# Kernel tuning notes

Measured on AMD Instinct MI355X. Metric: run time of the kernel, lower is better.

The kernel has to match this reference:

```python
import jax, jax.numpy as jnp
import numpy as np

H = 51  # num_hidden

def lstm_cell(x, h, c, Wih, Whh, bih, bhh):
    # PyTorch LSTMCell gate order: i, f, g, o
    gates = x @ Wih.T + bih + h @ Whh.T + bhh
    i, f, g, o = jnp.split(gates, 4, axis=-1)
    c_new = jax.nn.sigmoid(f) * c + jax.nn.sigmoid(i) * jnp.tanh(g)
    h_new = jax.nn.sigmoid(o) * jnp.tanh(c_new)
    return h_new, c_new

def setup_inputs() -> dict:
    key = jax.random.key(0)
    ks = jax.random.split(key, 9)
    B, T = 8192, 512
    s1 = 1.0 / np.sqrt(H)  # torch LSTMCell init scale U(-1/sqrt(H), 1/sqrt(H))
    s2 = 1.0
    u = lambda k, shape, s: jax.random.uniform(k, shape, jnp.float32, -s, s)
    return {
        "x": jax.random.normal(ks[0], (B, T), dtype=jnp.float32),
        "Wih1": u(ks[1], (4 * H, 1), s1),
        "Whh1": u(ks[2], (4 * H, H), s1),
        "bih1": u(ks[3], (4 * H,), s1),
        "bhh1": u(ks[4], (4 * H,), s1),
        "Wih2": u(ks[5], (4, H), s2),
        "Whh2": u(ks[6], (4, 1), s2),
        "bih2": u(ks[7], (4,), s2),
        "bhh2": u(ks[8], (4,), s2),
    }

def reference(x, Wih1, Whh1, bih1, bhh1, Wih2, Whh2, bih2, bhh2):
    B, T = x.shape
    xs = x.T[:, :, None]  # [T, B, 1]
    h1 = jnp.zeros((B, H), x.dtype)
    c1 = jnp.zeros((B, H), x.dtype)
    h2 = jnp.zeros((B, 1), x.dtype)
    c2 = jnp.zeros((B, 1), x.dtype)

    def step(carry, xt):
        h1, c1, h2, c2 = carry
        h1, c1 = lstm_cell(xt, h1, c1, Wih1, Whh1, bih1, bhh1)
        h2, c2 = lstm_cell(c1, h2, c2, Wih2, Whh2, bih2, bhh2)
        return (h1, c1, h2, c2), None

    (h1, c1, h2, c2), _ = jax.lax.scan(step, (h1, c1, h2, c2), xs)
    # extra step after the loop (as in the original forward)
    h1, c1 = lstm_cell(c2, h1, c1, Wih1, Whh1, bih1, bhh1)
    h2, output = lstm_cell(c1, h2, c2, Wih2, Whh2, bih2, bhh2)
    return output  # [B, 1] (final cell state of lstm2)
```

## Files before the change

### kernel.cpp

```cpp
#include <hip/hip_runtime.h>

#define TT 512
#define L2E  1.4426950408889634f
#define L2E2 2.8853900817779268f

typedef _Float16 f16;
typedef _Float16 f16x8 __attribute__((ext_vector_type(8)));
typedef float f32x4 __attribute__((ext_vector_type(4)));

__device__ __forceinline__ float fsig_p(float a){
    return __builtin_amdgcn_rcpf(1.f + __builtin_amdgcn_exp2f(-a));
}
__device__ __forceinline__ float ftanhg_p(float a){
    return 2.f * __builtin_amdgcn_rcpf(1.f + __builtin_amdgcn_exp2f(-a)) - 1.f;
}
__device__ __forceinline__ float ftanh_c(float c){
    return 2.f * __builtin_amdgcn_rcpf(1.f + __builtin_amdgcn_exp2f(-L2E2*c)) - 1.f;
}

#define FMA_LO(accv, wd, hh) asm("v_fma_mix_f32 %0, %1, %2, %0 op_sel:[0,0,0] op_sel_hi:[1,0,0]" : "+v"(accv) : "v"(wd), "v"(hh))
#define FMA_HI(accv, wd, hh) asm("v_fma_mix_f32 %0, %1, %2, %0 op_sel:[1,0,0] op_sel_hi:[1,0,0]" : "+v"(accv) : "v"(wd), "v"(hh))

__global__ void repack_w(const float* __restrict__ Whh1, const float* __restrict__ Wih1,
                         const float* __restrict__ bih1, const float* __restrict__ bhh1,
                         const float* __restrict__ Wih2,
                         f16* __restrict__ Wp, f16* __restrict__ Wp2)
{
    int i = blockIdx.x*256 + threadIdx.x;
    if (i < 13*2*64*8) {
        int b    = i & 7;
        int lane = (i >> 3) & 63;
        int kt   = (i >> 9) & 1;
        int m    = i >> 10;
        int r = m*16 + (lane & 15);
        int u = r >> 2, g = r & 3;
        int k = kt*32 + (lane >> 4)*8 + b;
        float v = 0.f;
        if (u < 51) {
            int rt = g*51 + u;
            if      (k < 51)  v = Whh1[rt*51 + k];
            else if (k == 51) v = Wih1[rt];
            else if (k == 52) v = bih1[rt] + bhh1[rt];
            v *= (g == 2) ? L2E2 : L2E;
        }
        Wp[i] = (f16)v;
    }
    if (i < 224) {
        int u = i >> 2, g = i & 3;
        float v = (u < 51) ? Wih2[g*51 + u] : 0.f;
        v *= (g == 2) ? L2E2 : L2E;
        Wp2[i] = (f16)v;
    }
}

__global__ __launch_bounds__(256, 2) void lstm_main(
    const float* __restrict__ X, const f16* __restrict__ Wp, const f16* __restrict__ Wp2,
    const float* __restrict__ Whh2, const float* __restrict__ bih2, const float* __restrict__ bhh2,
    float* __restrict__ out)
{
    __shared__ __align__(16) f16   HB[1024];
    __shared__ __align__(16) float PBL[4][16][4];
    __shared__ __align__(16) f16   HX[TT*16];

    const int tid  = threadIdx.x;
    const int w    = tid >> 6;
    const int lane = tid & 63;
    const int q    = (lane >> 4) & 3;
    const int jl   = lane & 15;
    const int d8   = jl & 7;
    const int bb   = blockIdx.x * 16;

    for (int i = tid; i < 512; i += 256) ((unsigned*)HB)[i] = 0u;
    if (tid < 256) ((unsigned*)PBL)[tid] = 0u;

    #pragma unroll
    for (int it = 0; it < 8; ++it) {
        int flat = it*1024 + tid*4;
        int row = flat >> 9, col = flat & 511;
        float4 v = *(const float4*)(X + (size_t)(bb + row)*TT + col);
        HX[(col+0)*16 + row] = (f16)v.x;
        HX[(col+1)*16 + row] = (f16)v.y;
        HX[(col+2)*16 + row] = (f16)v.z;
        HX[(col+3)*16 + row] = (f16)v.w;
    }
    __syncthreads();
    if (w == 0 && lane < 16) {
        int dd = lane & 7;
        HB[lane*64 + ((6 ^ dd) << 3) + 4] = (f16)1.f;
        HB[lane*64 + ((6 ^ dd) << 3) + 3] = HX[0*16 + lane];
    }

    const bool has4 = (w == 1);
    const int tiles[4] = {w, 4+w, 8+w, 12};
    f16x8 A0[4], A1[4];
    uint2 w2p[4];
    #pragma unroll
    for (int k = 0; k < 4; ++k) {
        int m = tiles[k];
        A0[k]  = *(const f16x8*)(Wp + (m*2+0)*512 + lane*8);
        A1[k]  = *(const f16x8*)(Wp + (m*2+1)*512 + lane*8);
        w2p[k] = *(const uint2*)(Wp2 + (m*4+q)*4);
    }
    float wh2[4], bs2[4];
    #pragma unroll
    for (int g = 0; g < 4; ++g) {
        float sc = (g == 2) ? L2E2 : L2E;
        wh2[g] = Whh2[g] * sc;
        bs2[g] = (bih2[g] + bhh2[g]) * sc;
    }

    float c1[4] = {0.f, 0.f, 0.f, 0.f};
    float c2 = 0.f, h2 = 0.f;
    const f32x4 zero4 = {0.f, 0.f, 0.f, 0.f};

    __syncthreads();

    for (int t = 0; t < TT; ++t) {
        const f16* rb = HB + jl*64;
        f16x8 B0 = *(const f16x8*)(rb + ((q       ^ d8) << 3));
        f16x8 B1 = *(const f16x8*)(rb + (((4 + q) ^ d8) << 3));

        f32x4 S0, S1, S2, S3;
        if (w == 3) {
            S0 = *(const f32x4*)&PBL[0][jl][0];
            S1 = *(const f32x4*)&PBL[1][jl][0];
            S2 = *(const f32x4*)&PBL[2][jl][0];
            S3 = *(const f32x4*)&PBL[3][jl][0];
        }

        __syncthreads();

        if (w == 3 && t > 0) {
            f32x4 S = S0 + S1 + S2 + S3;
            float g0 = S[0] + bs2[0] + wh2[0]*h2;
            float g1 = S[1] + bs2[1] + wh2[1]*h2;
            float g2 = S[2] + bs2[2] + wh2[2]*h2;
            float g3 = S[3] + bs2[3] + wh2[3]*h2;
            float i2 = fsig_p(g0), f2 = fsig_p(g1), gg2 = ftanhg_p(g2), o2 = fsig_p(g3);
            c2 = f2*c2 + i2*gg2;
            h2 = o2*ftanh_c(c2);
        }

        float p0 = 0.f, p1 = 0.f, p2 = 0.f, p3 = 0.f;
        #pragma unroll
        for (int k = 0; k < 4; ++k) {
            if (k < 3 || has4) {
                f32x4 a = __builtin_amdgcn_mfma_f32_16x16x32_f16(A0[k], B0, zero4, 0,0,0);
                a       = __builtin_amdgcn_mfma_f32_16x16x32_f16(A1[k], B1, a,     0,0,0);
                float ig = fsig_p(a[0]), fg = fsig_p(a[1]), gg = ftanhg_p(a[2]), og = fsig_p(a[3]);
                float c  = fg*c1[k] + ig*gg;
                c1[k] = c;
                int u = tiles[k]*4 + q;
                if (k < 3 || q < 3)
                    HB[jl*64 + (((u >> 3) ^ d8) << 3) + (u & 7)] = (f16)(og * ftanh_c(c));
                FMA_LO(p0, w2p[k].x, c); FMA_HI(p1, w2p[k].x, c);
                FMA_LO(p2, w2p[k].y, c); FMA_HI(p3, w2p[k].y, c);
            }
        }
        if (w == 0 && q == 3)
            HB[jl*64 + ((6 ^ d8) << 3) + 3] = HX[((t+1 < TT) ? t+1 : 0)*16 + jl];

        p0 += __shfl_xor(p0, 16); p0 += __shfl_xor(p0, 32);
        p1 += __shfl_xor(p1, 16); p1 += __shfl_xor(p1, 32);
        p2 += __shfl_xor(p2, 16); p2 += __shfl_xor(p2, 32);
        p3 += __shfl_xor(p3, 16); p3 += __shfl_xor(p3, 32);
        if (lane < 16) {
            f32x4 pv = {p0, p1, p2, p3};
            *(f32x4*)&PBL[w][jl][0] = pv;
        }
        __syncthreads();
    }

    if (w == 3) {
        f32x4 S = *(const f32x4*)&PBL[0][jl][0];
        S += *(const f32x4*)&PBL[1][jl][0];
        S += *(const f32x4*)&PBL[2][jl][0];
        S += *(const f32x4*)&PBL[3][jl][0];
        float g0 = S[0] + bs2[0] + wh2[0]*h2;
        float g1 = S[1] + bs2[1] + wh2[1]*h2;
        float g2 = S[2] + bs2[2] + wh2[2]*h2;
        float g3 = S[3] + bs2[3] + wh2[3]*h2;
        float i2 = fsig_p(g0), f2 = fsig_p(g1), gg2 = ftanhg_p(g2), o2 = fsig_p(g3);
        c2 = f2*c2 + i2*gg2;
        h2 = o2*ftanh_c(c2);
        if (lane < 16) HB[jl*64 + ((6 ^ d8) << 3) + 3] = (f16)c2;
    }
    __syncthreads();

    {
        const f16* rb = HB + jl*64;
        f16x8 B0 = *(const f16x8*)(rb + ((q       ^ d8) << 3));
        f16x8 B1 = *(const f16x8*)(rb + (((4 + q) ^ d8) << 3));

        float p0 = 0.f, p1 = 0.f, p2 = 0.f, p3 = 0.f;
        #pragma unroll
        for (int k = 0; k < 4; ++k) {
            if (k < 3 || has4) {
                f32x4 a = __builtin_amdgcn_mfma_f32_16x16x32_f16(A0[k], B0, zero4, 0,0,0);
                a       = __builtin_amdgcn_mfma_f32_16x16x32_f16(A1[k], B1, a,     0,0,0);
                float ig = fsig_p(a[0]), fg = fsig_p(a[1]), gg = ftanhg_p(a[2]);
                float c  = fg*c1[k] + ig*gg;
                FMA_LO(p0, w2p[k].x, c); FMA_HI(p1, w2p[k].x, c);
                FMA_LO(p2, w2p[k].y, c); FMA_HI(p3, w2p[k].y, c);
            }
        }
        p0 += __shfl_xor(p0, 16); p0 += __shfl_xor(p0, 32);
        p1 += __shfl_xor(p1, 16); p1 += __shfl_xor(p1, 32);
        p2 += __shfl_xor(p2, 16); p2 += __shfl_xor(p2, 32);
        p3 += __shfl_xor(p3, 16); p3 += __shfl_xor(p3, 32);
        if (lane < 16) {
            f32x4 pv = {p0, p1, p2, p3};
            *(f32x4*)&PBL[w][jl][0] = pv;
        }
    }
    __syncthreads();

    if (w == 3) {
        f32x4 S = *(const f32x4*)&PBL[0][jl][0];
        S += *(const f32x4*)&PBL[1][jl][0];
        S += *(const f32x4*)&PBL[2][jl][0];
        S += *(const f32x4*)&PBL[3][jl][0];
        float g0 = S[0] + bs2[0] + wh2[0]*h2;
        float g1 = S[1] + bs2[1] + wh2[1]*h2;
        float g2 = S[2] + bs2[2] + wh2[2]*h2;
        float i2 = fsig_p(g0), f2 = fsig_p(g1), gg2 = ftanhg_p(g2);
        float c2n = f2*c2 + i2*gg2;
        if (lane < 16) out[bb + jl] = c2n;
    }
}

extern "C" void kernel_launch(void* const* d_in, const int* in_sizes, int n_in,
                              void* d_out, int out_size, void* d_ws, size_t ws_size,
                              hipStream_t stream) {
    const float* X    = (const float*)d_in[0];
    const float* Wih1 = (const float*)d_in[1];
    const float* Whh1 = (const float*)d_in[2];
    const float* bih1 = (const float*)d_in[3];
    const float* bhh1 = (const float*)d_in[4];
    const float* Wih2 = (const float*)d_in[5];
    const float* Whh2 = (const float*)d_in[6];
    const float* bih2 = (const float*)d_in[7];
    const float* bhh2 = (const float*)d_in[8];
    float* out = (float*)d_out;

    f16* Wp  = (f16*)d_ws;
    f16* Wp2 = (f16*)((char*)d_ws + 26624);

    repack_w<<<52, 256, 0, stream>>>(Whh1, Wih1, bih1, bhh1, Wih2, Wp, Wp2);
    lstm_main<<<512, 256, 0, stream>>>(X, Wp, Wp2, Whh2, bih2, bhh2, out);
}
```

Before: 435.5 us.

## Double-buffer LSTM hidden state and partials to drop one barrier per step

Hidden-state and layer-2 partial-sum buffers in shared memory become ping-pong buffers, so each timestep reads one parity and writes the other. This removes the mid-step __syncthreads. Tile assignment is also rebalanced so wave 3, which runs the layer-2 cell, gets fewer MFMA tiles while waves 0 and 1 take four, and wave 3 now writes the next input. The cost is double the LDS for these buffers and more complex indexing.

```diff
diff --git a/kernel.cpp b/kernel.cpp
--- a/kernel.cpp
+++ b/kernel.cpp
@@ -58,8 +58,8 @@
     const float* __restrict__ Whh2, const float* __restrict__ bih2, const float* __restrict__ bhh2,
     float* __restrict__ out)
 {
-    __shared__ __align__(16) f16   HB[1024];
-    __shared__ __align__(16) float PBL[4][16][4];
+    __shared__ __align__(16) f16   HB[2048];
+    __shared__ __align__(16) float PBL[2][4][16][4];
     __shared__ __align__(16) f16   HX[TT*16];
 
     const int tid  = threadIdx.x;
@@ -70,8 +70,8 @@
     const int d8   = jl & 7;
     const int bb   = blockIdx.x * 16;
 
-    for (int i = tid; i < 512; i += 256) ((unsigned*)HB)[i] = 0u;
-    if (tid < 256) ((unsigned*)PBL)[tid] = 0u;
+    for (int i = tid; i < 1024; i += 256) ((unsigned*)HB)[i] = 0u;
+    for (int i = tid; i < 512;  i += 256) ((unsigned*)PBL)[i] = 0u;
 
     #pragma unroll
     for (int it = 0; it < 8; ++it) {
@@ -86,17 +86,19 @@
     __syncthreads();
     if (w == 0 && lane < 16) {
         int dd = lane & 7;
-        HB[lane*64 + ((6 ^ dd) << 3) + 4] = (f16)1.f;
-        HB[lane*64 + ((6 ^ dd) << 3) + 3] = HX[0*16 + lane];
-    }
-
-    const bool has4 = (w == 1);
-    const int tiles[4] = {w, 4+w, 8+w, 12};
+        HB[       lane*64 + ((6 ^ dd) << 3) + 4] = (f16)1.f;
+        HB[1024 + lane*64 + ((6 ^ dd) << 3) + 4] = (f16)1.f;
+        HB[       lane*64 + ((6 ^ dd) << 3) + 3] = HX[0*16 + lane];
+    }
+
+    const int NT = (w <= 1) ? 4 : (w == 2 ? 3 : 2);
+    const int t3 = (w == 0) ? 12 : (w == 1 ? 11 : 0);
+    const int tiles[4] = { w, 4+w, 8+w, t3 };
     f16x8 A0[4], A1[4];
     uint2 w2p[4];
     #pragma unroll
     for (int k = 0; k < 4; ++k) {
-        int m = tiles[k];
+        int m = (k < NT) ? tiles[k] : 0;
         A0[k]  = *(const f16x8*)(Wp + (m*2+0)*512 + lane*8);
         A1[k]  = *(const f16x8*)(Wp + (m*2+1)*512 + lane*8);
         w2p[k] = *(const uint2*)(Wp2 + (m*4+q)*4);
@@ -116,49 +118,49 @@
     __syncthreads();
 
     for (int t = 0; t < TT; ++t) {
-        const f16* rb = HB + jl*64;
+        const int rp = t & 1;
+        const f16* rb = HB + rp*1024 + jl*64;
         f16x8 B0 = *(const f16x8*)(rb + ((q       ^ d8) << 3));
         f16x8 B1 = *(const f16x8*)(rb + (((4 + q) ^ d8) << 3));
 
         f32x4 S0, S1, S2, S3;
+        f16 xn;
         if (w == 3) {
-            S0 = *(const f32x4*)&PBL[0][jl][0];
-            S1 = *(const f32x4*)&PBL[1][jl][0];
-            S2 = *(const f32x4*)&PBL[2][jl][0];
-            S3 = *(const f32x4*)&PBL[3][jl][0];
-        }
-
-        __syncthreads();
-
-        if (w == 3 && t > 0) {
-            f32x4 S = S0 + S1 + S2 + S3;
-            float g0 = S[0] + bs2[0] + wh2[0]*h2;
-            float g1 = S[1] + bs2[1] + wh2[1]*h2;
-            float g2 = S[2] + bs2[2] + wh2[2]*h2;
-            float g3 = S[3] + bs2[3] + wh2[3]*h2;
-            float i2 = fsig_p(g0), f2 = fsig_p(g1), gg2 = ftanhg_p(g2), o2 = fsig_p(g3);
-            c2 = f2*c2 + i2*gg2;
-            h2 = o2*ftanh_c(c2);
+            S0 = *(const f32x4*)&PBL[rp][0][jl][0];
+            S1 = *(const f32x4*)&PBL[rp][1][jl][0];
+            S2 = *(const f32x4*)&PBL[rp][2][jl][0];
+            S3 = *(const f32x4*)&PBL[rp][3][jl][0];
+            xn = HX[((t+1 < TT) ? t+1 : 0)*16 + jl];
+            if (t > 0) {
+                f32x4 S = S0 + S1 + S2 + S3;
+                float g0 = S[0] + bs2[0] + wh2[0]*h2;
+                float g1 = S[1] + bs2[1] + wh2[1]*h2;
+                float g2 = S[2] + bs2[2] + wh2[2]*h2;
+                float g3 = S[3] + bs2[3] + wh2[3]*h2;
+                float i2 = fsig_p(g0), f2 = fsig_p(g1), gg2 = ftanhg_p(g2), o2 = fsig_p(g3);
+                c2 = f2*c2 + i2*gg2;
+                h2 = o2*ftanh_c(c2);
+            }
         }
 
         float p0 = 0.f, p1 = 0.f, p2 = 0.f, p3 = 0.f;
         #pragma unroll
         for (int k = 0; k < 4; ++k) {
-            if (k < 3 || has4) {
+            if (k < NT) {
                 f32x4 a = __builtin_amdgcn_mfma_f32_16x16x32_f16(A0[k], B0, zero4, 0,0,0);
                 a       = __builtin_amdgcn_mfma_f32_16x16x32_f16(A1[k], B1, a,     0,0,0);
                 float ig = fsig_p(a[0]), fg = fsig_p(a[1]), gg = ftanhg_p(a[2]), og = fsig_p(a[3]);
                 float c  = fg*c1[k] + ig*gg;
                 c1[k] = c;
                 int u = tiles[k]*4 + q;
-                if (k < 3 || q < 3)
-                    HB[jl*64 + (((u >> 3) ^ d8) << 3) + (u & 7)] = (f16)(og * ftanh_c(c));
+                if (u < 51)
+                    HB[(rp^1)*1024 + jl*64 + (((u >> 3) ^ d8) << 3) + (u & 7)] = (f16)(og * ftanh_c(c));
                 FMA_LO(p0, w2p[k].x, c); FMA_HI(p1, w2p[k].x, c);
                 FMA_LO(p2, w2p[k].y, c); FMA_HI(p3, w2p[k].y, c);
             }
         }
-        if (w == 0 && q == 3)
-            HB[jl*64 + ((6 ^ d8) << 3) + 3] = HX[((t+1 < TT) ? t+1 : 0)*16 + jl];
+        if (w == 3 && q == 3)
+            HB[(rp^1)*1024 + jl*64 + ((6 ^ d8) << 3) + 3] = xn;
 
         p0 += __shfl_xor(p0, 16); p0 += __shfl_xor(p0, 32);
         p1 += __shfl_xor(p1, 16); p1 += __shfl_xor(p1, 32);
@@ -166,16 +168,16 @@
         p3 += __shfl_xor(p3, 16); p3 += __shfl_xor(p3, 32);
         if (lane < 16) {
             f32x4 pv = {p0, p1, p2, p3};
-            *(f32x4*)&PBL[w][jl][0] = pv;
+            *(f32x4*)&PBL[rp^1][w][jl][0] = pv;
         }
         __syncthreads();
     }
 
     if (w == 3) {
-        f32x4 S = *(const f32x4*)&PBL[0][jl][0];
-        S += *(const f32x4*)&PBL[1][jl][0];
-        S += *(const f32x4*)&PBL[2][jl][0];
-        S += *(const f32x4*)&PBL[3][jl][0];
+        f32x4 S = *(const f32x4*)&PBL[0][0][jl][0];
+        S += *(const f32x4*)&PBL[0][1][jl][0];
+        S += *(const f32x4*)&PBL[0][2][jl][0];
+        S += *(const f32x4*)&PBL[0][3][jl][0];
         float g0 = S[0] + bs2[0] + wh2[0]*h2;
         float g1 = S[1] + bs2[1] + wh2[1]*h2;
         float g2 = S[2] + bs2[2] + wh2[2]*h2;
@@ -195,7 +197,7 @@
         float p0 = 0.f, p1 = 0.f, p2 = 0.f, p3 = 0.f;
         #pragma unroll
         for (int k = 0; k < 4; ++k) {
-            if (k < 3 || has4) {
+            if (k < NT) {
                 f32x4 a = __builtin_amdgcn_mfma_f32_16x16x32_f16(A0[k], B0, zero4, 0,0,0);
                 a       = __builtin_amdgcn_mfma_f32_16x16x32_f16(A1[k], B1, a,     0,0,0);
                 float ig = fsig_p(a[0]), fg = fsig_p(a[1]), gg = ftanhg_p(a[2]);
@@ -210,16 +212,16 @@
         p3 += __shfl_xor(p3, 16); p3 += __shfl_xor(p3, 32);
         if (lane < 16) {
             f32x4 pv = {p0, p1, p2, p3};
-            *(f32x4*)&PBL[w][jl][0] = pv;
+            *(f32x4*)&PBL[1][w][jl][0] = pv;
         }
     }
     __syncthreads();
 
     if (w == 3) {
-        f32x4 S = *(const f32x4*)&PBL[0][jl][0];
-        S += *(const f32x4*)&PBL[1][jl][0];
-        S += *(const f32x4*)&PBL[2][jl][0];
-        S += *(const f32x4*)&PBL[3][jl][0];
+        f32x4 S = *(const f32x4*)&PBL[1][0][jl][0];
+        S += *(const f32x4*)&PBL[1][1][jl][0];
+        S += *(const f32x4*)&PBL[1][2][jl][0];
+        S += *(const f32x4*)&PBL[1][3][jl][0];
         float g0 = S[0] + bs2[0] + wh2[0]*h2;
         float g1 = S[1] + bs2[1] + wh2[1]*h2;
         float g2 = S[2] + bs2[2] + wh2[2]*h2;
```

Result: slower. 478.2 us (+9.8%).

## Offload LSTM2 cell update and x injection to a dedicated fifth wavefront

Applied to the files above, without the earlier changes.

Adds a fifth wavefront per block that handles the second LSTM cell's update and writes the next input into the hidden buffer. Wave 3 previously did this serial work on top of its own layer-1 tiles, lengthening the critical path of each timestep. The two chained MFMAs are also split into independent ones whose results are summed, which shortens the dependency chain. In exchange there are more threads per block and more barrier participants, which may lower occupancy.

```diff
diff --git a/kernel.cpp b/kernel.cpp
--- a/kernel.cpp
+++ b/kernel.cpp
@@ -3,6 +3,7 @@
 #define TT 512
 #define L2E  1.4426950408889634f
 #define L2E2 2.8853900817779268f
+#define NTHR 320
 
 typedef _Float16 f16;
 typedef _Float16 f16x8 __attribute__((ext_vector_type(8)));
@@ -53,7 +54,7 @@
     }
 }
 
-__global__ __launch_bounds__(256, 2) void lstm_main(
+__global__ __launch_bounds__(NTHR, 2) void lstm_main(
     const float* __restrict__ X, const f16* __restrict__ Wp, const f16* __restrict__ Wp2,
     const float* __restrict__ Whh2, const float* __restrict__ bih2, const float* __restrict__ bhh2,
     float* __restrict__ out)
@@ -70,12 +71,10 @@
     const int d8   = jl & 7;
     const int bb   = blockIdx.x * 16;
 
-    for (int i = tid; i < 512; i += 256) ((unsigned*)HB)[i] = 0u;
-    if (tid < 256) ((unsigned*)PBL)[tid] = 0u;
-
-    #pragma unroll
-    for (int it = 0; it < 8; ++it) {
-        int flat = it*1024 + tid*4;
+    for (int i = tid; i < 512; i += NTHR) ((unsigned*)HB)[i] = 0u;
+    for (int i = tid; i < 256; i += NTHR) ((unsigned*)PBL)[i] = 0u;
+
+    for (int flat = tid*4; flat < 8192; flat += NTHR*4) {
         int row = flat >> 9, col = flat & 511;
         float4 v = *(const float4*)(X + (size_t)(bb + row)*TT + col);
         HX[(col+0)*16 + row] = (f16)v.x;
@@ -90,8 +89,9 @@
         HB[lane*64 + ((6 ^ dd) << 3) + 3] = HX[0*16 + lane];
     }
 
+    const int wv   = (w < 4) ? w : 0;
     const bool has4 = (w == 1);
-    const int tiles[4] = {w, 4+w, 8+w, 12};
+    const int tiles[4] = { wv, 4+wv, 8+wv, 12 };
     f16x8 A0[4], A1[4];
     uint2 w2p[4];
     #pragma unroll
@@ -116,62 +116,67 @@
     __syncthreads();
 
     for (int t = 0; t < TT; ++t) {
-        const f16* rb = HB + jl*64;
-        f16x8 B0 = *(const f16x8*)(rb + ((q       ^ d8) << 3));
-        f16x8 B1 = *(const f16x8*)(rb + (((4 + q) ^ d8) << 3));
-
+        f16x8 B0, B1;
         f32x4 S0, S1, S2, S3;
-        if (w == 3) {
+        f16 xn;
+        if (w < 4) {
+            const f16* rb = HB + jl*64;
+            B0 = *(const f16x8*)(rb + ((q       ^ d8) << 3));
+            B1 = *(const f16x8*)(rb + (((4 + q) ^ d8) << 3));
+        } else {
             S0 = *(const f32x4*)&PBL[0][jl][0];
             S1 = *(const f32x4*)&PBL[1][jl][0];
             S2 = *(const f32x4*)&PBL[2][jl][0];
             S3 = *(const f32x4*)&PBL[3][jl][0];
+            xn = HX[((t+1 < TT) ? t+1 : 0)*16 + jl];
         }
 
         __syncthreads();
 
-        if (w == 3 && t > 0) {
-            f32x4 S = S0 + S1 + S2 + S3;
-            float g0 = S[0] + bs2[0] + wh2[0]*h2;
-            float g1 = S[1] + bs2[1] + wh2[1]*h2;
-            float g2 = S[2] + bs2[2] + wh2[2]*h2;
-            float g3 = S[3] + bs2[3] + wh2[3]*h2;
-            float i2 = fsig_p(g0), f2 = fsig_p(g1), gg2 = ftanhg_p(g2), o2 = fsig_p(g3);
-            c2 = f2*c2 + i2*gg2;
-            h2 = o2*ftanh_c(c2);
-        }
-
-        float p0 = 0.f, p1 = 0.f, p2 = 0.f, p3 = 0.f;
-        #pragma unroll
-        for (int k = 0; k < 4; ++k) {
-            if (k < 3 || has4) {
-                f32x4 a = __builtin_amdgcn_mfma_f32_16x16x32_f16(A0[k], B0, zero4, 0,0,0);
-                a       = __builtin_amdgcn_mfma_f32_16x16x32_f16(A1[k], B1, a,     0,0,0);
-                float ig = fsig_p(a[0]), fg = fsig_p(a[1]), gg = ftanhg_p(a[2]), og = fsig_p(a[3]);
-                float c  = fg*c1[k] + ig*gg;
-                c1[k] = c;
-                int u = tiles[k]*4 + q;
-                if (k < 3 || q < 3)
-                    HB[jl*64 + (((u >> 3) ^ d8) << 3) + (u & 7)] = (f16)(og * ftanh_c(c));
-                FMA_LO(p0, w2p[k].x, c); FMA_HI(p1, w2p[k].x, c);
-                FMA_LO(p2, w2p[k].y, c); FMA_HI(p3, w2p[k].y, c);
-            }
-        }
-        if (w == 0 && q == 3)
-            HB[jl*64 + ((6 ^ d8) << 3) + 3] = HX[((t+1 < TT) ? t+1 : 0)*16 + jl];
-
-        p0 += __shfl_xor(p0, 16); p0 += __shfl_xor(p0, 32);
-        p1 += __shfl_xor(p1, 16); p1 += __shfl_xor(p1, 32);
-        p2 += __shfl_xor(p2, 16); p2 += __shfl_xor(p2, 32);
-        p3 += __shfl_xor(p3, 16); p3 += __shfl_xor(p3, 32);
-        if (lane < 16) {
-            f32x4 pv = {p0, p1, p2, p3};
-            *(f32x4*)&PBL[w][jl][0] = pv;
+        if (w == 4) {
+            if (t > 0) {
+                f32x4 S = S0 + S1 + S2 + S3;
+                float g0 = S[0] + bs2[0] + wh2[0]*h2;
+                float g1 = S[1] + bs2[1] + wh2[1]*h2;
+                float g2 = S[2] + bs2[2] + wh2[2]*h2;
+                float g3 = S[3] + bs2[3] + wh2[3]*h2;
+                float i2 = fsig_p(g0), f2 = fsig_p(g1), gg2 = ftanhg_p(g2), o2 = fsig_p(g3);
+                c2 = f2*c2 + i2*gg2;
+                h2 = o2*ftanh_c(c2);
+            }
+            if (lane < 16)
+                HB[jl*64 + ((6 ^ d8) << 3) + 3] = xn;
+        } else {
+            float p0 = 0.f, p1 = 0.f, p2 = 0.f, p3 = 0.f;
+            #pragma unroll
+            for (int k = 0; k < 4; ++k) {
+                if (k < 3 || has4) {
+                    f32x4 a  = __builtin_amdgcn_mfma_f32_16x16x32_f16(A0[k], B0, zero4, 0,0,0);
+                    f32x4 a2 = __builtin_amdgcn_mfma_f32_16x16x32_f16(A1[k], B1, zero4, 0,0,0);
+                    a += a2;
+                    float ig = fsig_p(a[0]), fg = fsig_p(a[1]), gg = ftanhg_p(a[2]), og = fsig_p(a[3]);
+                    float c  = fg*c1[k] + ig*gg;
+                    c1[k] = c;
+                    int u = tiles[k]*4 + q;
+                    if (k < 3 || q < 3)
+                        HB[jl*64 + (((u >> 3) ^ d8) << 3) + (u & 7)] = (f16)(og * ftanh_c(c));
+                    FMA_LO(p0, w2p[k].x, c); FMA_HI(p1, w2p[k].x, c);
+                    FMA_LO(p2, w2p[k].y, c); FMA_HI(p3, w2p[k].y, c);
+                }
+            }
+            p0 += __shfl_xor(p0, 16); p0 += __shfl_xor(p0, 32);
+            p1 += __shfl_xor(p1, 16); p1 += __shfl_xor(p1, 32);
+            p2 += __shfl_xor(p2, 16); p2 += __shfl_xor(p2, 32);
+            p3 += __shfl_xor(p3, 16); p3 += __shfl_xor(p3, 32);
+            if (lane < 16) {
+                f32x4 pv = {p0, p1, p2, p3};
+                *(f32x4*)&PBL[w][jl][0] = pv;
+            }
         }
         __syncthreads();
     }
 
-    if (w == 3) {
+    if (w == 4) {
         f32x4 S = *(const f32x4*)&PBL[0][jl][0];
         S += *(const f32x4*)&PBL[1][jl][0];
         S += *(const f32x4*)&PBL[2][jl][0];
@@ -187,7 +192,7 @@
     }
     __syncthreads();
 
-    {
+    if (w < 4) {
         const f16* rb = HB + jl*64;
         f16x8 B0 = *(const f16x8*)(rb + ((q       ^ d8) << 3));
         f16x8 B1 = *(const f16x8*)(rb + (((4 + q) ^ d8) << 3));
@@ -196,8 +201,9 @@
         #pragma unroll
         for (int k = 0; k < 4; ++k) {
             if (k < 3 || has4) {
-                f32x4 a = __builtin_amdgcn_mfma_f32_16x16x32_f16(A0[k], B0, zero4, 0,0,0);
-                a       = __builtin_amdgcn_mfma_f32_16x16x32_f16(A1[k], B1, a,     0,0,0);
+                f32x4 a  = __builtin_amdgcn_mfma_f32_16x16x32_f16(A0[k], B0, zero4, 0,0,0);
+                f32x4 a2 = __builtin_amdgcn_mfma_f32_16x16x32_f16(A1[k], B1, zero4, 0,0,0);
+                a += a2;
                 float ig = fsig_p(a[0]), fg = fsig_p(a[1]), gg = ftanhg_p(a[2]);
                 float c  = fg*c1[k] + ig*gg;
                 FMA_LO(p0, w2p[k].x, c); FMA_HI(p1, w2p[k].x, c);
@@ -215,7 +221,7 @@
     }
     __syncthreads();
 
-    if (w == 3) {
+    if (w == 4) {
         f32x4 S = *(const f32x4*)&PBL[0][jl][0];
         S += *(const f32x4*)&PBL[1][jl][0];
         S += *(const f32x4*)&PBL[2][jl][0];
@@ -247,5 +253,5 @@
     f16* Wp2 = (f16*)((char*)d_ws + 26624);
 
     repack_w<<<52, 256, 0, stream>>>(Whh1, Wih1, bih1, bhh1, Wih2, Wp, Wp2);
-    lstm_main<<<512, 256, 0, stream>>>(X, Wp, Wp2, Whh2, bih2, bhh2, out);
-}
+    lstm_main<<<512, NTHR, 0, stream>>>(X, Wp, Wp2, Whh2, bih2, bhh2, out);
+}
```

Measured after the change: 489.1 us. 1.12x slower.
